# Performance work log

Measured on AMD Instinct MI355X. Metric: run time of the kernel, lower is better.

## Reference

```python
import jax, jax.numpy as jnp
import numpy as np

H = 1024
V = 32000
S = 2048


def _lstm_cell(x, h_prev, c_prev, W_ih, W_hh, b_ih, b_hh):
    # PyTorch gate order: input, forget, cell(g), output
    gates = x @ W_ih.T + b_ih + h_prev @ W_hh.T + b_hh  # (1, 4H)
    i, f, g, o = jnp.split(gates, 4, axis=-1)
    i = jax.nn.sigmoid(i)
    f = jax.nn.sigmoid(f)
    g = jnp.tanh(g)
    o = jax.nn.sigmoid(o)
    c_new = f * c_prev + i * g
    h_new = o * jnp.tanh(c_new)
    return h_new, c_new


def setup_inputs() -> dict:
    key = jax.random.key(0)
    ks = jax.random.split(key, 16)
    sc = 0.05
    inp = {
        "input_ids": jax.random.randint(ks[0], (1,), 0, V, dtype=jnp.int64) if jax.config.jax_enable_x64 else jax.random.randint(ks[0], (1,), 0, V, dtype=jnp.int32),
        "h": jax.random.normal(ks[1], (2, 1, H), jnp.float32),
        "c": jax.random.normal(ks[2], (2, 1, H), jnp.float32),
        "encoder_outputs": jax.random.normal(ks[3], (S, H), jnp.float32),
        "embedding": jax.random.normal(ks[4], (V, H), jnp.float32) * sc,
        "W_ih0": jax.random.normal(ks[5], (4 * H, H), jnp.float32) * sc,
        "W_hh0": jax.random.normal(ks[6], (4 * H, H), jnp.float32) * sc,
        "b_ih0": jax.random.normal(ks[7], (4 * H,), jnp.float32) * sc,
        "b_hh0": jax.random.normal(ks[8], (4 * H,), jnp.float32) * sc,
        "W_ih1": jax.random.normal(ks[9], (4 * H, H), jnp.float32) * sc,
        "W_hh1": jax.random.normal(ks[10], (4 * H, H), jnp.float32) * sc,
        "b_ih1": jax.random.normal(ks[11], (4 * H,), jnp.float32) * sc,
        "b_hh1": jax.random.normal(ks[12], (4 * H,), jnp.float32) * sc,
        "W_out": jax.random.normal(ks[13], (V, H), jnp.float32) * sc,
        "b_out": jax.random.normal(ks[14], (V,), jnp.float32) * sc,
    }
    return inp


def reference(input_ids, h, c, encoder_outputs, embedding,
              W_ih0, W_hh0, b_ih0, b_hh0,
              W_ih1, W_hh1, b_ih1, b_hh1,
              W_out, b_out):
    # embedding lookup; dropout is identity in eval mode
    x = embedding[input_ids[0]][None, :]                      # (1, H)

    # attention: scores against layer-0 hidden state
    scores = encoder_outputs @ h[0, 0]                        # (S,)
    attn_w = jax.nn.softmax(scores)                           # (S,)
    ctx = attn_w @ encoder_outputs                            # (H,) attention_applied
    ctx_h = ctx[None, :]                                      # (1, H)

    # custom hidden-state injection: both layers' h replaced by context
    h0, c0 = _lstm_cell(x, ctx_h, c[0], W_ih0, W_hh0, b_ih0, b_hh0)
    h1, c1 = _lstm_cell(h0, ctx_h, c[1], W_ih1, W_hh1, b_ih1, b_hh1)

    logits = h1 @ W_out.T + b_out                             # (1, V)
    h_new = jnp.stack([h0, h1])                               # (2, 1, H)
    c_new = jnp.stack([c0, c1])                               # (2, 1, H)
    return logits, h_new, c_new, attn_w[None, :]
```

## Files before the change

### kernel.cpp

```cpp
#include <hip/hip_runtime.h>

#define HH 1024
#define VV 32000
#define SS 2048

__device__ __forceinline__ float wave_sum64(float v) {
    #pragma unroll
    for (int off = 32; off; off >>= 1) v += __shfl_down(v, off, 64);
    return v;
}

__device__ __forceinline__ float sigmoidf(float x) {
    return 1.f / (1.f + expf(-x));
}

__global__ __launch_bounds__(256) void scores_kernel(
    const float* __restrict__ E, const float* __restrict__ h,
    float* __restrict__ scores, float* __restrict__ ctx) {
    int wave = (blockIdx.x * blockDim.x + threadIdx.x) >> 6;
    int lane = threadIdx.x & 63;
    if (blockIdx.x == 0) {
        ((float4*)ctx)[threadIdx.x] = make_float4(0.f, 0.f, 0.f, 0.f);
    }
    const float4* Er = (const float4*)(E + (size_t)wave * HH);
    const float4* hv = (const float4*)h;
    float acc = 0.f;
    #pragma unroll
    for (int k = 0; k < 4; ++k) {
        float4 e = Er[lane + 64 * k];
        float4 x = hv[lane + 64 * k];
        acc += e.x * x.x + e.y * x.y + e.z * x.z + e.w * x.w;
    }
    acc = wave_sum64(acc);
    if (lane == 0) scores[wave] = acc;
}

__global__ __launch_bounds__(256) void softmax_ctx_kernel(
    const float* __restrict__ E, const float* __restrict__ scores,
    float* __restrict__ attn_out, float* __restrict__ ctx) {
    __shared__ float red[4];
    __shared__ float s_max, s_sum;
    __shared__ float w[16];
    int t = threadIdx.x;
    float4 a = ((const float4*)scores)[t];
    float4 b = ((const float4*)scores)[t + 256];
    float m = fmaxf(fmaxf(fmaxf(a.x, a.y), fmaxf(a.z, a.w)),
                    fmaxf(fmaxf(b.x, b.y), fmaxf(b.z, b.w)));
    #pragma unroll
    for (int off = 32; off; off >>= 1) m = fmaxf(m, __shfl_xor(m, off, 64));
    if ((t & 63) == 0) red[t >> 6] = m;
    __syncthreads();
    if (t == 0) s_max = fmaxf(fmaxf(red[0], red[1]), fmaxf(red[2], red[3]));
    __syncthreads();
    float sm = s_max;
    float sum = expf(a.x - sm) + expf(a.y - sm) + expf(a.z - sm) + expf(a.w - sm)
              + expf(b.x - sm) + expf(b.y - sm) + expf(b.z - sm) + expf(b.w - sm);
    sum = wave_sum64(sum);
    if ((t & 63) == 0) red[t >> 6] = sum;
    __syncthreads();
    if (t == 0) s_sum = red[0] + red[1] + red[2] + red[3];
    __syncthreads();
    float inv = 1.f / s_sum;
    int rowBase = blockIdx.x * 16;
    if (t < 16) {
        float aw = expf(scores[rowBase + t] - sm) * inv;
        w[t] = aw;
        attn_out[rowBase + t] = aw;
    }
    __syncthreads();
    float4 acc = make_float4(0.f, 0.f, 0.f, 0.f);
    #pragma unroll
    for (int s = 0; s < 16; ++s) {
        float ws_ = w[s];
        float4 e = ((const float4*)(E + (size_t)(rowBase + s) * HH))[t];
        acc.x += ws_ * e.x; acc.y += ws_ * e.y; acc.z += ws_ * e.z; acc.w += ws_ * e.w;
    }
    atomicAdd(&ctx[4 * t + 0], acc.x);
    atomicAdd(&ctx[4 * t + 1], acc.y);
    atomicAdd(&ctx[4 * t + 2], acc.z);
    atomicAdd(&ctx[4 * t + 3], acc.w);
}

__global__ __launch_bounds__(256) void gates0_kernel(
    const float* __restrict__ Wih, const float* __restrict__ Whh,
    const float* __restrict__ bih, const float* __restrict__ bhh,
    const float* __restrict__ emb, const int* __restrict__ ids,
    const float* __restrict__ ctx, float* __restrict__ gates) {
    int wave = (blockIdx.x * blockDim.x + threadIdx.x) >> 6;
    int lane = threadIdx.x & 63;
    const float* x = emb + (size_t)ids[0] * HH;
    const float4* A  = (const float4*)(Wih + (size_t)wave * HH);
    const float4* B  = (const float4*)(Whh + (size_t)wave * HH);
    const float4* xv = (const float4*)x;
    const float4* hv = (const float4*)ctx;
    float acc = 0.f;
    #pragma unroll
    for (int k = 0; k < 4; ++k) {
        float4 aa = A[lane + 64 * k];
        float4 xx = xv[lane + 64 * k];
        acc += aa.x * xx.x + aa.y * xx.y + aa.z * xx.z + aa.w * xx.w;
        float4 bb = B[lane + 64 * k];
        float4 hh = hv[lane + 64 * k];
        acc += bb.x * hh.x + bb.y * hh.y + bb.z * hh.z + bb.w * hh.w;
    }
    acc = wave_sum64(acc);
    if (lane == 0) gates[wave] = acc + bih[wave] + bhh[wave];
}

__global__ __launch_bounds__(256) void lstm1_gates_kernel(
    const float* __restrict__ Wih, const float* __restrict__ Whh,
    const float* __restrict__ bih, const float* __restrict__ bhh,
    const float* __restrict__ gates0, const float* __restrict__ c0_in,
    const float* __restrict__ ctx,
    float* __restrict__ h0_out, float* __restrict__ c0_out,
    float* __restrict__ gates1) {
    __shared__ float4 hs[256];
    int t = threadIdx.x;
    {
        float4 gi = ((const float4*)(gates0       ))[t];
        float4 gf = ((const float4*)(gates0 + 1024))[t];
        float4 gg = ((const float4*)(gates0 + 2048))[t];
        float4 go = ((const float4*)(gates0 + 3072))[t];
        float4 cp = ((const float4*)c0_in)[t];
        float4 c4, h4;
        c4.x = sigmoidf(gf.x) * cp.x + sigmoidf(gi.x) * tanhf(gg.x);
        c4.y = sigmoidf(gf.y) * cp.y + sigmoidf(gi.y) * tanhf(gg.y);
        c4.z = sigmoidf(gf.z) * cp.z + sigmoidf(gi.z) * tanhf(gg.z);
        c4.w = sigmoidf(gf.w) * cp.w + sigmoidf(gi.w) * tanhf(gg.w);
        h4.x = sigmoidf(go.x) * tanhf(c4.x);
        h4.y = sigmoidf(go.y) * tanhf(c4.y);
        h4.z = sigmoidf(go.z) * tanhf(c4.z);
        h4.w = sigmoidf(go.w) * tanhf(c4.w);
        hs[t] = h4;
        if (blockIdx.x == 0) {
            ((float4*)h0_out)[t] = h4;
            ((float4*)c0_out)[t] = c4;
        }
    }
    __syncthreads();
    int row  = blockIdx.x * 4 + (t >> 6);
    int lane = t & 63;
    const float4* A  = (const float4*)(Wih + (size_t)row * HH);
    const float4* B  = (const float4*)(Whh + (size_t)row * HH);
    const float4* hv = (const float4*)hs;
    const float4* cv = (const float4*)ctx;
    float acc = 0.f;
    #pragma unroll
    for (int k = 0; k < 4; ++k) {
        float4 aa = A[lane + 64 * k];
        float4 xx = hv[lane + 64 * k];
        acc += aa.x * xx.x + aa.y * xx.y + aa.z * xx.z + aa.w * xx.w;
        float4 bb = B[lane + 64 * k];
        float4 hh = cv[lane + 64 * k];
        acc += bb.x * hh.x + bb.y * hh.y + bb.z * hh.z + bb.w * hh.w;
    }
    acc = wave_sum64(acc);
    if (lane == 0) gates1[row] = acc + bih[row] + bhh[row];
}

__global__ __launch_bounds__(256) void logits_fused_kernel(
    const float* __restrict__ W, const float* __restrict__ bout,
    const float* __restrict__ gates1, const float* __restrict__ c1_in,
    float* __restrict__ h1_out, float* __restrict__ c1_out,
    float* __restrict__ out) {
    __shared__ float4 hs[256];
    int t = threadIdx.x;
    {
        float4 gi = ((const float4*)(gates1       ))[t];
        float4 gf = ((const float4*)(gates1 + 1024))[t];
        float4 gg = ((const float4*)(gates1 + 2048))[t];
        float4 go = ((const float4*)(gates1 + 3072))[t];
        float4 cp = ((const float4*)c1_in)[t];
        float4 c4, h4;
        c4.x = sigmoidf(gf.x) * cp.x + sigmoidf(gi.x) * tanhf(gg.x);
        c4.y = sigmoidf(gf.y) * cp.y + sigmoidf(gi.y) * tanhf(gg.y);
        c4.z = sigmoidf(gf.z) * cp.z + sigmoidf(gi.z) * tanhf(gg.z);
        c4.w = sigmoidf(gf.w) * cp.w + sigmoidf(gi.w) * tanhf(gg.w);
        h4.x = sigmoidf(go.x) * tanhf(c4.x);
        h4.y = sigmoidf(go.y) * tanhf(c4.y);
        h4.z = sigmoidf(go.z) * tanhf(c4.z);
        h4.w = sigmoidf(go.w) * tanhf(c4.w);
        hs[t] = h4;
        if (blockIdx.x == 0) {
            ((float4*)h1_out)[t] = h4;
            ((float4*)c1_out)[t] = c4;
        }
    }
    __syncthreads();
    int row  = blockIdx.x * 4 + (t >> 6);
    int lane = t & 63;
    const float4* Wr = (const float4*)(W + (size_t)row * HH);
    const float4* hv = (const float4*)hs;
    float acc = 0.f;
    #pragma unroll
    for (int k = 0; k < 4; ++k) {
        float4 w4 = Wr[lane + 64 * k];
        float4 x4 = hv[lane + 64 * k];
        acc += w4.x * x4.x + w4.y * x4.y + w4.z * x4.z + w4.w * x4.w;
    }
    acc = wave_sum64(acc);
    if (lane == 0) out[row] = acc + bout[row];
}

extern "C" void kernel_launch(void* const* d_in, const int* in_sizes, int n_in,
                              void* d_out, int out_size, void* d_ws, size_t ws_size,
                              hipStream_t stream) {
    const int*   ids   = (const int*)  d_in[0];
    const float* h_in  = (const float*)d_in[1];
    const float* c_in  = (const float*)d_in[2];
    const float* E     = (const float*)d_in[3];
    const float* emb   = (const float*)d_in[4];
    const float* Wih0  = (const float*)d_in[5];
    const float* Whh0  = (const float*)d_in[6];
    const float* bih0  = (const float*)d_in[7];
    const float* bhh0  = (const float*)d_in[8];
    const float* Wih1  = (const float*)d_in[9];
    const float* Whh1  = (const float*)d_in[10];
    const float* bih1  = (const float*)d_in[11];
    const float* bhh1  = (const float*)d_in[12];
    const float* Wout  = (const float*)d_in[13];
    const float* bout  = (const float*)d_in[14];

    float* out = (float*)d_out;
    float* logits   = out;
    float* h0_out   = out + 32000;
    float* h1_out   = out + 33024;
    float* c0_out   = out + 34048;
    float* c1_out   = out + 35072;
    float* attn_out = out + 36096;

    float* ws = (float*)d_ws;
    float* scores  = ws;
    float* ctx     = ws + 2048;
    float* gates0  = ws + 3072;
    float* gates1  = ws + 7168;

    scores_kernel<<<512, 256, 0, stream>>>(E, h_in, scores, ctx);
    softmax_ctx_kernel<<<128, 256, 0, stream>>>(E, scores, attn_out, ctx);
    gates0_kernel<<<1024, 256, 0, stream>>>(Wih0, Whh0, bih0, bhh0,
                                            emb, ids, ctx, gates0);
    lstm1_gates_kernel<<<1024, 256, 0, stream>>>(Wih1, Whh1, bih1, bhh1,
                                                 gates0, c_in, ctx,
                                                 h0_out, c0_out, gates1);
    logits_fused_kernel<<<8000, 256, 0, stream>>>(Wout, bout, gates1, c_in + 1024,
                                                  h1_out, c1_out, logits);
}
```

Baseline: 68.99 us.

## Restructure LSTM pipeline: hoist ctx-independent GEMVs, prefetch weights before gate math

```diff
diff --git a/kernel.cpp b/kernel.cpp
--- a/kernel.cpp
+++ b/kernel.cpp
@@ -9,30 +9,41 @@
     for (int off = 32; off; off >>= 1) v += __shfl_down(v, off, 64);
     return v;
 }
-
-__device__ __forceinline__ float sigmoidf(float x) {
-    return 1.f / (1.f + expf(-x));
-}
-
-__global__ __launch_bounds__(256) void scores_kernel(
+__device__ __forceinline__ float sigmoidf(float x) { return 1.f / (1.f + expf(-x)); }
+__device__ __forceinline__ float dot4(float4 a, float4 b) {
+    return a.x * b.x + a.y * b.y + a.z * b.z + a.w * b.w;
+}
+
+__global__ __launch_bounds__(256) void k1_scores_g0(
     const float* __restrict__ E, const float* __restrict__ h,
-    float* __restrict__ scores, float* __restrict__ ctx) {
-    int wave = (blockIdx.x * blockDim.x + threadIdx.x) >> 6;
-    int lane = threadIdx.x & 63;
-    if (blockIdx.x == 0) {
-        ((float4*)ctx)[threadIdx.x] = make_float4(0.f, 0.f, 0.f, 0.f);
-    }
-    const float4* Er = (const float4*)(E + (size_t)wave * HH);
+    const float* __restrict__ Wih0, const float* __restrict__ bih0,
+    const float* __restrict__ bhh0,
+    const float* __restrict__ emb, const int* __restrict__ ids,
+    float* __restrict__ scores, float* __restrict__ g0, float* __restrict__ ctx) {
+    int tid = threadIdx.x;
+    int w = (blockIdx.x * 256 + tid) >> 6;
+    int lane = tid & 63;
+    if (blockIdx.x == 0) ((float4*)ctx)[tid] = make_float4(0.f, 0.f, 0.f, 0.f);
+
     const float4* hv = (const float4*)h;
-    float acc = 0.f;
-    #pragma unroll
-    for (int k = 0; k < 4; ++k) {
-        float4 e = Er[lane + 64 * k];
-        float4 x = hv[lane + 64 * k];
-        acc += e.x * x.x + e.y * x.y + e.z * x.z + e.w * x.w;
-    }
+    float4 h0 = hv[lane], h1 = hv[lane + 64], h2 = hv[lane + 128], h3 = hv[lane + 192];
+    const float4* Er = (const float4*)(E + (size_t)w * HH);
+    float acc = dot4(Er[lane], h0) + dot4(Er[lane + 64], h1)
+              + dot4(Er[lane + 128], h2) + dot4(Er[lane + 192], h3);
     acc = wave_sum64(acc);
-    if (lane == 0) scores[wave] = acc;
+    if (lane == 0) scores[w] = acc;
+
+    const float4* xv = (const float4*)(emb + (size_t)ids[0] * HH);
+    float4 x0 = xv[lane], x1 = xv[lane + 64], x2 = xv[lane + 128], x3 = xv[lane + 192];
+    #pragma unroll
+    for (int t = 0; t < 2; ++t) {
+        int row = w + t * 2048;
+        const float4* Wr = (const float4*)(Wih0 + (size_t)row * HH);
+        float a = dot4(Wr[lane], x0) + dot4(Wr[lane + 64], x1)
+                + dot4(Wr[lane + 128], x2) + dot4(Wr[lane + 192], x3);
+        a = wave_sum64(a);
+        if (lane == 0) g0[row] = a + bih0[row] + bhh0[row];
+    }
 }
 
 __global__ __launch_bounds__(256) void softmax_ctx_kernel(
@@ -81,47 +92,44 @@
     atomicAdd(&ctx[4 * t + 3], acc.w);
 }
 
-__global__ __launch_bounds__(256) void gates0_kernel(
-    const float* __restrict__ Wih, const float* __restrict__ Whh,
-    const float* __restrict__ bih, const float* __restrict__ bhh,
-    const float* __restrict__ emb, const int* __restrict__ ids,
-    const float* __restrict__ ctx, float* __restrict__ gates) {
-    int wave = (blockIdx.x * blockDim.x + threadIdx.x) >> 6;
-    int lane = threadIdx.x & 63;
-    const float* x = emb + (size_t)ids[0] * HH;
-    const float4* A  = (const float4*)(Wih + (size_t)wave * HH);
-    const float4* B  = (const float4*)(Whh + (size_t)wave * HH);
-    const float4* xv = (const float4*)x;
-    const float4* hv = (const float4*)ctx;
-    float acc = 0.f;
-    #pragma unroll
-    for (int k = 0; k < 4; ++k) {
-        float4 aa = A[lane + 64 * k];
-        float4 xx = xv[lane + 64 * k];
-        acc += aa.x * xx.x + aa.y * xx.y + aa.z * xx.z + aa.w * xx.w;
-        float4 bb = B[lane + 64 * k];
-        float4 hh = hv[lane + 64 * k];
-        acc += bb.x * hh.x + bb.y * hh.y + bb.z * hh.z + bb.w * hh.w;
-    }
-    acc = wave_sum64(acc);
-    if (lane == 0) gates[wave] = acc + bih[wave] + bhh[wave];
-}
-
-__global__ __launch_bounds__(256) void lstm1_gates_kernel(
-    const float* __restrict__ Wih, const float* __restrict__ Whh,
-    const float* __restrict__ bih, const float* __restrict__ bhh,
-    const float* __restrict__ gates0, const float* __restrict__ c0_in,
-    const float* __restrict__ ctx,
-    float* __restrict__ h0_out, float* __restrict__ c0_out,
-    float* __restrict__ gates1) {
+__global__ __launch_bounds__(256) void k3_whh(
+    const float* __restrict__ Whh0, const float* __restrict__ Whh1,
+    const float* __restrict__ bih1, const float* __restrict__ bhh1,
+    const float* __restrict__ ctx, float* __restrict__ g0, float* __restrict__ g1) {
+    int tid = threadIdx.x;
+    int w = (blockIdx.x * 256 + tid) >> 6;
+    int lane = tid & 63;
+    const float4* cv = (const float4*)ctx;
+    float4 c0 = cv[lane], c1 = cv[lane + 64], c2 = cv[lane + 128], c3 = cv[lane + 192];
+    const float4* W0 = (const float4*)(Whh0 + (size_t)w * HH);
+    float a = dot4(W0[lane], c0) + dot4(W0[lane + 64], c1)
+            + dot4(W0[lane + 128], c2) + dot4(W0[lane + 192], c3);
+    a = wave_sum64(a);
+    const float4* W1 = (const float4*)(Whh1 + (size_t)w * HH);
+    float b = dot4(W1[lane], c0) + dot4(W1[lane + 64], c1)
+            + dot4(W1[lane + 128], c2) + dot4(W1[lane + 192], c3);
+    b = wave_sum64(b);
+    if (lane == 0) {
+        g0[w] += a;
+        g1[w] = b + bih1[w] + bhh1[w];
+    }
+}
+
+__global__ __launch_bounds__(256) void k4_gates1(
+    const float* __restrict__ Wih1, const float* __restrict__ g0,
+    const float* __restrict__ c0_in, float* __restrict__ g1,
+    float* __restrict__ h0_out, float* __restrict__ c0_out) {
     __shared__ float4 hs[256];
-    int t = threadIdx.x;
+    int tid = threadIdx.x, warp = tid >> 6, lane = tid & 63;
+    int row0 = blockIdx.x * 8 + warp * 2;
+    const float4* Wr = (const float4*)(Wih1 + (size_t)row0 * HH);
+    float4 a0 = Wr[lane], a1 = Wr[lane + 64], a2 = Wr[lane + 128], a3 = Wr[lane + 192];
     {
-        float4 gi = ((const float4*)(gates0       ))[t];
-        float4 gf = ((const float4*)(gates0 + 1024))[t];
-        float4 gg = ((const float4*)(gates0 + 2048))[t];
-        float4 go = ((const float4*)(gates0 + 3072))[t];
-        float4 cp = ((const float4*)c0_in)[t];
+        float4 gi = ((const float4*)(g0       ))[tid];
+        float4 gf = ((const float4*)(g0 + 1024))[tid];
+        float4 gg = ((const float4*)(g0 + 2048))[tid];
+        float4 go = ((const float4*)(g0 + 3072))[tid];
+        float4 cp = ((const float4*)c0_in)[tid];
         float4 c4, h4;
         c4.x = sigmoidf(gf.x) * cp.x + sigmoidf(gi.x) * tanhf(gg.x);
         c4.y = sigmoidf(gf.y) * cp.y + sigmoidf(gi.y) * tanhf(gg.y);
@@ -131,46 +139,40 @@
         h4.y = sigmoidf(go.y) * tanhf(c4.y);
         h4.z = sigmoidf(go.z) * tanhf(c4.z);
         h4.w = sigmoidf(go.w) * tanhf(c4.w);
-        hs[t] = h4;
+        hs[tid] = h4;
         if (blockIdx.x == 0) {
-            ((float4*)h0_out)[t] = h4;
-            ((float4*)c0_out)[t] = c4;
+            ((float4*)h0_out)[tid] = h4;
+            ((float4*)c0_out)[tid] = c4;
         }
     }
     __syncthreads();
-    int row  = blockIdx.x * 4 + (t >> 6);
-    int lane = t & 63;
-    const float4* A  = (const float4*)(Wih + (size_t)row * HH);
-    const float4* B  = (const float4*)(Whh + (size_t)row * HH);
-    const float4* hv = (const float4*)hs;
-    const float4* cv = (const float4*)ctx;
-    float acc = 0.f;
-    #pragma unroll
-    for (int k = 0; k < 4; ++k) {
-        float4 aa = A[lane + 64 * k];
-        float4 xx = hv[lane + 64 * k];
-        acc += aa.x * xx.x + aa.y * xx.y + aa.z * xx.z + aa.w * xx.w;
-        float4 bb = B[lane + 64 * k];
-        float4 hh = cv[lane + 64 * k];
-        acc += bb.x * hh.x + bb.y * hh.y + bb.z * hh.z + bb.w * hh.w;
-    }
-    acc = wave_sum64(acc);
-    if (lane == 0) gates1[row] = acc + bih[row] + bhh[row];
-}
-
-__global__ __launch_bounds__(256) void logits_fused_kernel(
+    float4 x0 = hs[lane], x1 = hs[lane + 64], x2 = hs[lane + 128], x3 = hs[lane + 192];
+    float acc0 = dot4(a0, x0) + dot4(a1, x1) + dot4(a2, x2) + dot4(a3, x3);
+    acc0 = wave_sum64(acc0);
+    if (lane == 0) g1[row0] += acc0;
+    const float4* W2 = Wr + 256;
+    float acc1 = dot4(W2[lane], x0) + dot4(W2[lane + 64], x1)
+               + dot4(W2[lane + 128], x2) + dot4(W2[lane + 192], x3);
+    acc1 = wave_sum64(acc1);
+    if (lane == 0) g1[row0 + 1] += acc1;
+}
+
+__global__ __launch_bounds__(256) void k5_logits(
     const float* __restrict__ W, const float* __restrict__ bout,
-    const float* __restrict__ gates1, const float* __restrict__ c1_in,
+    const float* __restrict__ g1, const float* __restrict__ c1_in,
     float* __restrict__ h1_out, float* __restrict__ c1_out,
     float* __restrict__ out) {
     __shared__ float4 hs[256];
-    int t = threadIdx.x;
+    int tid = threadIdx.x, warp = tid >> 6, lane = tid & 63;
+    int row0 = blockIdx.x * 32 + warp * 8;
+    const float4* Wr = (const float4*)(W + (size_t)row0 * HH);
+    float4 a0 = Wr[lane], a1 = Wr[lane + 64], a2 = Wr[lane + 128], a3 = Wr[lane + 192];
     {
-        float4 gi = ((const float4*)(gates1       ))[t];
-        float4 gf = ((const float4*)(gates1 + 1024))[t];
-        float4 gg = ((const float4*)(gates1 + 2048))[t];
-        float4 go = ((const float4*)(gates1 + 3072))[t];
-        float4 cp = ((const float4*)c1_in)[t];
+        float4 gi = ((const float4*)(g1       ))[tid];
+        float4 gf = ((const float4*)(g1 + 1024))[tid];
+        float4 gg = ((const float4*)(g1 + 2048))[tid];
+        float4 go = ((const float4*)(g1 + 3072))[tid];
+        float4 cp = ((const float4*)c1_in)[tid];
         float4 c4, h4;
         c4.x = sigmoidf(gf.x) * cp.x + sigmoidf(gi.x) * tanhf(gg.x);
         c4.y = sigmoidf(gf.y) * cp.y + sigmoidf(gi.y) * tanhf(gg.y);
@@ -180,26 +182,26 @@
         h4.y = sigmoidf(go.y) * tanhf(c4.y);
         h4.z = sigmoidf(go.z) * tanhf(c4.z);
         h4.w = sigmoidf(go.w) * tanhf(c4.w);
-        hs[t] = h4;
+        hs[tid] = h4;
         if (blockIdx.x == 0) {
-            ((float4*)h1_out)[t] = h4;
-            ((float4*)c1_out)[t] = c4;
+            ((float4*)h1_out)[tid] = h4;
+            ((float4*)c1_out)[tid] = c4;
         }
     }
     __syncthreads();
-    int row  = blockIdx.x * 4 + (t >> 6);
-    int lane = t & 63;
-    const float4* Wr = (const float4*)(W + (size_t)row * HH);
-    const float4* hv = (const float4*)hs;
-    float acc = 0.f;
-    #pragma unroll
-    for (int k = 0; k < 4; ++k) {
-        float4 w4 = Wr[lane + 64 * k];
-        float4 x4 = hv[lane + 64 * k];
-        acc += w4.x * x4.x + w4.y * x4.y + w4.z * x4.z + w4.w * x4.w;
-    }
-    acc = wave_sum64(acc);
-    if (lane == 0) out[row] = acc + bout[row];
+    float4 x0 = hs[lane], x1 = hs[lane + 64], x2 = hs[lane + 128], x3 = hs[lane + 192];
+    #pragma unroll
+    for (int i = 0; i < 8; ++i) {
+        float4 b0 = a0, b1 = a1, b2 = a2, b3 = a3;
+        if (i < 7) {
+            const float4* Nx = Wr + (i + 1) * 256;
+            b0 = Nx[lane]; b1 = Nx[lane + 64]; b2 = Nx[lane + 128]; b3 = Nx[lane + 192];
+        }
+        float acc = dot4(a0, x0) + dot4(a1, x1) + dot4(a2, x2) + dot4(a3, x3);
+        acc = wave_sum64(acc);
+        if (lane == 0) out[row0 + i] = acc + bout[row0 + i];
+        a0 = b0; a1 = b1; a2 = b2; a3 = b3;
+    }
 }
 
 extern "C" void kernel_launch(void* const* d_in, const int* in_sizes, int n_in,
@@ -230,18 +232,16 @@
     float* attn_out = out + 36096;
 
     float* ws = (float*)d_ws;
-    float* scores  = ws;
-    float* ctx     = ws + 2048;
-    float* gates0  = ws + 3072;
-    float* gates1  = ws + 7168;
-
-    scores_kernel<<<512, 256, 0, stream>>>(E, h_in, scores, ctx);
+    float* scores = ws;
+    float* ctx    = ws + 2048;
+    float* g0     = ws + 3072;
+    float* g1     = ws + 7168;
+
+    k1_scores_g0<<<512, 256, 0, stream>>>(E, h_in, Wih0, bih0, bhh0,
+                                          emb, ids, scores, g0, ctx);
     softmax_ctx_kernel<<<128, 256, 0, stream>>>(E, scores, attn_out, ctx);
-    gates0_kernel<<<1024, 256, 0, stream>>>(Wih0, Whh0, bih0, bhh0,
-                                            emb, ids, ctx, gates0);
-    lstm1_gates_kernel<<<1024, 256, 0, stream>>>(Wih1, Whh1, bih1, bhh1,
-                                                 gates0, c_in, ctx,
-                                                 h0_out, c0_out, gates1);
-    logits_fused_kernel<<<8000, 256, 0, stream>>>(Wout, bout, gates1, c_in + 1024,
-                                                  h1_out, c1_out, logits);
-}
+    k3_whh<<<1024, 256, 0, stream>>>(Whh0, Whh1, bih1, bhh1, ctx, g0, g1);
+    k4_gates1<<<512, 256, 0, stream>>>(Wih1, g0, c_in, g1, h0_out, c0_out);
+    k5_logits<<<1000, 256, 0, stream>>>(Wout, bout, g1, c_in + 1024,
+                                        h1_out, c1_out, logits);
+}
```

New measurement: 60.45 us. 1.14x faster.
